# Performance work log

Measured on AMD Instinct MI355X. Metric: run time of the kernel, lower is better.

The kernel has to match this reference:

```python
import jax, jax.numpy as jnp
import numpy as np

N_NODES = 50000
N_EDGES = 800000
NUM_FEATS = 512
NUM_CLASSES = 64
NUM_LAYERS = 4


def setup_inputs() -> dict:
    key = jax.random.key(0)
    k1, k2, k3 = jax.random.split(key, 3)
    x = jax.random.normal(k1, (N_NODES, NUM_FEATS), dtype=jnp.float32)
    # glorot init for weight [num_feats, num_classes]
    scale = jnp.sqrt(6.0 / (NUM_FEATS + NUM_CLASSES)).astype(jnp.float32)
    weight = jax.random.uniform(k2, (NUM_FEATS, NUM_CLASSES), dtype=jnp.float32,
                                minval=-scale, maxval=scale)
    edge_index = jax.random.randint(k3, (2, N_EDGES), 0, N_NODES, dtype=jnp.int64)
    return {"x": x, "weight": weight, "edge_index": edge_index}


def reference(x, weight, edge_index):
    row, col = edge_index[0], edge_index[1]  # [E], [E]
    # symmetric GCN normalization: deg^{-1/2}[row] * deg^{-1/2}[col]
    deg = jax.ops.segment_sum(jnp.ones((edge_index.shape[1],), dtype=x.dtype),
                              row, num_segments=x.shape[0])  # [N]
    deg_inv_sqrt = jnp.where(deg > 0, jax.lax.rsqrt(jnp.maximum(deg, 1e-12)), 0.0)
    norm = (deg_inv_sqrt[row] * deg_inv_sqrt[col])[:, None]  # [E, 1]

    h = x @ weight  # [N, num_classes] (dropout skipped: eval mode)
    for _ in range(NUM_LAYERS):
        # gather source features, scale by edge norm, scatter-add to destinations
        msg = norm * h[row]  # [E, num_classes]
        h = jax.ops.segment_sum(msg, col, num_segments=x.shape[0])  # [N, num_classes]
        # type_norm == 'None' -> layers_bn is identity
    return h
```

## Files before the change

kernel.cpp:

```cpp
#include <hip/hip_runtime.h>
#include <hip/hip_fp16.h>

#define NFEAT 512
#define NCLS  64
#define NNODES 50000
#define NW    (NNODES / 4)
#define NB    256
#define SLOTS 64

typedef unsigned int uint;
using short8 = __attribute__((ext_vector_type(8))) short;
using f32x4  = __attribute__((ext_vector_type(4))) float;

static __device__ __forceinline__ unsigned short f32_to_bf16_rne(float f) {
    unsigned u = __float_as_uint(f);
    unsigned r = u + 0x7FFFu + ((u >> 16) & 1u);
    return (unsigned short)(r >> 16);
}
static __device__ __forceinline__ float bf16_to_f32(unsigned short b) {
    return __uint_as_float(((unsigned)b) << 16);
}
static __device__ __forceinline__ uint cvt_pk_bf16(float a, float b) {
    uint r;
    asm("v_cvt_pk_bf16_f32 %0, %1, %2" : "=v"(r) : "v"(a), "v"(b));
    return r;
}
static __device__ __forceinline__ void split_bf16x8(const float* xs, short8& ahi, short8& alo) {
    union { uint u[4]; short8 s; } H, L;
#pragma unroll
    for (int t = 0; t < 4; ++t) {
        float x0 = xs[2 * t], x1 = xs[2 * t + 1];
        uint hp = cvt_pk_bf16(x0, x1);
        float f0 = __uint_as_float(hp << 16);
        float f1 = __uint_as_float(hp & 0xffff0000u);
        uint lp = cvt_pk_bf16(x0 - f0, x1 - f1);
        H.u[t] = hp; L.u[t] = lp;
    }
    ahi = H.s; alo = L.s;
}


__global__ __launch_bounds__(256) void hist_packw_kernel(
        const int* __restrict__ row, const int* __restrict__ col,
        const float* __restrict__ w,
        uint* __restrict__ degB, uint* __restrict__ cntB,
        short8* __restrict__ wp, int E, int CH) {
    __shared__ __align__(16) uint h[2 * NW];
    int b = blockIdx.x;
    if (b < NB) {
        for (int i = threadIdx.x; i < 2 * NW; i += 256) h[i] = 0;
        __syncthreads();
        int e0 = b * CH, e1 = min(E, e0 + CH);
        for (int e = e0 + threadIdx.x; e < e1; e += 256) {
            int c = col[e], r = row[e];
            atomicAdd(&h[c >> 2], 1u << ((c & 3) * 8));
            atomicAdd(&h[NW + (r >> 2)], 1u << ((r & 3) * 8));
        }
        __syncthreads();
        uint4* cb = reinterpret_cast<uint4*>(cntB + (size_t)b * NW);
        uint4* db = reinterpret_cast<uint4*>(degB + (size_t)b * NW);
        const uint4* c4 = reinterpret_cast<const uint4*>(h);
        const uint4* d4 = reinterpret_cast<const uint4*>(h + NW);
        for (int i = threadIdx.x; i < NW / 4; i += 256) cb[i] = c4[i];
        for (int i = threadIdx.x; i < NW / 4; i += 256) db[i] = d4[i];
        return;
    }
    int gid = (b - NB) * 256 + threadIdx.x;
    int lane = gid & 63;
    int F = gid >> 6;
    int s = F & 1;
    int nt = (F >> 1) & 3;
    int kk = F >> 3;
    int k0 = kk * 32 + (lane >> 4) * 8;
    int c  = nt * 16 + (lane & 15);
    short8 v;
#pragma unroll
    for (int j = 0; j < 8; ++j) {
        float xv = w[(k0 + j) * NCLS + c];
        unsigned short hi = f32_to_bf16_rne(xv);
        unsigned short outv = hi;
        if (s) outv = f32_to_bf16_rne(xv - bf16_to_f32(hi));
        v[j] = (short)outv;
    }
    wp[gid] = v;
}


__global__ __launch_bounds__(256) void reduce_kernel(uint* __restrict__ cntB,
                                                     const uint* __restrict__ degB,
                                                     int* __restrict__ cntTot,
                                                     float* __restrict__ dinv) {
    int gid = blockIdx.x * 256 + threadIdx.x;
    if (gid < NW) {
        int wi = gid;
        uint run = 0;
#pragma unroll 8
        for (int b = 0; b < NB; ++b) {
            uint v = cntB[(size_t)b * NW + wi];
            cntB[(size_t)b * NW + wi] = run;
            run += v;
        }
        int4 t = { (int)(run & 255), (int)((run >> 8) & 255),
                   (int)((run >> 16) & 255), (int)(run >> 24) };
        *reinterpret_cast<int4*>(cntTot + wi * 4) = t;
    } else if (gid < 2 * NW) {
        int wi = gid - NW;
        uint run = 0;
#pragma unroll 8
        for (int b = 0; b < NB; ++b) run += degB[(size_t)b * NW + wi];
        int d0 = run & 255, d1 = (run >> 8) & 255, d2 = (run >> 16) & 255, d3 = run >> 24;
        float4 dv;
        dv.x = d0 ? rsqrtf((float)d0) : 0.0f;
        dv.y = d1 ? rsqrtf((float)d1) : 0.0f;
        dv.z = d2 ? rsqrtf((float)d2) : 0.0f;
        dv.w = d3 ? rsqrtf((float)d3) : 0.0f;
        *reinterpret_cast<float4*>(dinv + wi * 4) = dv;
    }
}


__global__ __launch_bounds__(256, 2) void place_matmul_kernel(
        const int* __restrict__ row, const int* __restrict__ col,
        const uint* __restrict__ offB, int* __restrict__ slots,
        const float* __restrict__ x, const short8* __restrict__ wp,
        const float* __restrict__ dinv, __half* __restrict__ u0,
        int N, int E, int CH) {
    __shared__ __align__(16) uint sh[NW];
    int b = blockIdx.x;

    if (b < NB) {
        uint4* c4 = reinterpret_cast<uint4*>(sh);
        const uint4* o4 = reinterpret_cast<const uint4*>(offB + (size_t)b * NW);
        for (int i = threadIdx.x; i < NW / 4; i += 256) c4[i] = o4[i];
        __syncthreads();
        int e0 = b * CH, e1 = min(E, e0 + CH);
        for (int e = e0 + threadIdx.x; e < e1; e += 256) {
            int c = col[e];
            uint old = atomicAdd(&sh[c >> 2], 1u << ((c & 3) * 8));
            int pos = (old >> ((c & 3) * 8)) & 255;
            if (pos < SLOTS) slots[(c << 6) + pos] = row[e];
        }
        return;
    }

    int tile = b - NB;
    int tid = threadIdx.x;
    int wave = tid >> 6, lane = tid & 63;
    int rlo = lane & 15, khi = lane >> 4;
    int row0 = tile * 128 + wave * 32;

    size_t roff[2];
#pragma unroll
    for (int rg = 0; rg < 2; ++rg) {
        int rr = row0 + rg * 16 + rlo;
        if (rr > N - 1) rr = N - 1;
        roff[rg] = (size_t)rr * NFEAT + khi * 8;
    }

    f32x4 acc[2][4];
#pragma unroll
    for (int rg = 0; rg < 2; ++rg)
#pragma unroll
        for (int nt = 0; nt < 4; ++nt) acc[rg][nt] = f32x4{0.f, 0.f, 0.f, 0.f};

    const short8* fbase = wp + lane;
    for (int ch = 0; ch < 4; ++ch) {
#pragma unroll
        for (int kk = 0; kk < 4; ++kk) {
            const short8* fb = fbase + ch * 2048 + kk * 512;
            short8 bh0 = fb[0],   bl0 = fb[64];
            short8 bh1 = fb[128], bl1 = fb[192];
            short8 bh2 = fb[256], bl2 = fb[320];
            short8 bh3 = fb[384], bl3 = fb[448];
            int kg = ch * 128 + kk * 32;
#pragma unroll
            for (int rg = 0; rg < 2; ++rg) {
                float4 xa = *reinterpret_cast<const float4*>(x + roff[rg] + kg);
                float4 xb = *reinterpret_cast<const float4*>(x + roff[rg] + kg + 4);
                float xs[8] = {xa.x, xa.y, xa.z, xa.w, xb.x, xb.y, xb.z, xb.w};
                short8 ahi, alo;
                split_bf16x8(xs, ahi, alo);
                acc[rg][0] = __builtin_amdgcn_mfma_f32_16x16x32_bf16(ahi, bh0, acc[rg][0], 0, 0, 0);
                acc[rg][1] = __builtin_amdgcn_mfma_f32_16x16x32_bf16(ahi, bh1, acc[rg][1], 0, 0, 0);
                acc[rg][2] = __builtin_amdgcn_mfma_f32_16x16x32_bf16(ahi, bh2, acc[rg][2], 0, 0, 0);
                acc[rg][3] = __builtin_amdgcn_mfma_f32_16x16x32_bf16(ahi, bh3, acc[rg][3], 0, 0, 0);
                acc[rg][0] = __builtin_amdgcn_mfma_f32_16x16x32_bf16(alo, bh0, acc[rg][0], 0, 0, 0);
                acc[rg][1] = __builtin_amdgcn_mfma_f32_16x16x32_bf16(alo, bh1, acc[rg][1], 0, 0, 0);
                acc[rg][2] = __builtin_amdgcn_mfma_f32_16x16x32_bf16(alo, bh2, acc[rg][2], 0, 0, 0);
                acc[rg][3] = __builtin_amdgcn_mfma_f32_16x16x32_bf16(alo, bh3, acc[rg][3], 0, 0, 0);
                acc[rg][0] = __builtin_amdgcn_mfma_f32_16x16x32_bf16(ahi, bl0, acc[rg][0], 0, 0, 0);
                acc[rg][1] = __builtin_amdgcn_mfma_f32_16x16x32_bf16(ahi, bl1, acc[rg][1], 0, 0, 0);
                acc[rg][2] = __builtin_amdgcn_mfma_f32_16x16x32_bf16(ahi, bl2, acc[rg][2], 0, 0, 0);
                acc[rg][3] = __builtin_amdgcn_mfma_f32_16x16x32_bf16(ahi, bl3, acc[rg][3], 0, 0, 0);
            }
        }
    }

#pragma unroll
    for (int rg = 0; rg < 2; ++rg) {
        int rbase = row0 + rg * 16 + khi * 4;
#pragma unroll
        for (int j = 0; j < 4; ++j) {
            int r = rbase + j;
            if (r < N) {
                float dn = dinv[r];
                __half* op = u0 + ((size_t)r << 6) + rlo;
                op[0]  = __float2half(acc[rg][0][j] * dn);
                op[16] = __float2half(acc[rg][1][j] * dn);
                op[32] = __float2half(acc[rg][2][j] * dn);
                op[48] = __float2half(acc[rg][3][j] * dn);
            }
        }
    }
}


__global__ __launch_bounds__(256) void gather_kernel(const __half* __restrict__ u,
                                                     const int* __restrict__ cntTot,
                                                     const int* __restrict__ slots,
                                                     const float* __restrict__ dinv,
                                                     __half* __restrict__ out_h,
                                                     float* __restrict__ out_f,
                                                     int N, int sq) {
    int wid = blockIdx.x * 4 + (threadIdx.x >> 6);
    if (wid >= N) return;
    int lane = threadIdx.x & 63;
    int q = lane >> 3;
    int p = lane & 7;
    int cq = cntTot[wid];
    cq = (cq < SLOTS) ? cq : SLOTS;
    const int* sl = slots + (wid << 6);
    int s_l = sl[lane];

    float a0=0.f,a1=0.f,a2=0.f,a3=0.f,a4=0.f,a5=0.f,a6=0.f,a7=0.f;
    float b0=0.f,b1=0.f,b2=0.f,b3=0.f,b4=0.f,b5=0.f,b6=0.f,b7=0.f;
#pragma unroll
    for (int j = 0; j < 8; j += 2) {
        int i0 = q + 8 * j;
        int i1 = q + 8 * (j + 1);
        int s0 = __shfl(s_l, i0);
        int s1 = __shfl(s_l, i1);
        if (i0 < cq) {
            uint4 d0 = *reinterpret_cast<const uint4*>(u + ((size_t)s0 << 6) + p * 8);
            float2 f0 = __half22float2(*reinterpret_cast<__half2*>(&d0.x));
            float2 f1 = __half22float2(*reinterpret_cast<__half2*>(&d0.y));
            float2 f2 = __half22float2(*reinterpret_cast<__half2*>(&d0.z));
            float2 f3 = __half22float2(*reinterpret_cast<__half2*>(&d0.w));
            a0 += f0.x; a1 += f0.y; a2 += f1.x; a3 += f1.y;
            a4 += f2.x; a5 += f2.y; a6 += f3.x; a7 += f3.y;
        }
        if (i1 < cq) {
            uint4 d1 = *reinterpret_cast<const uint4*>(u + ((size_t)s1 << 6) + p * 8);
            float2 g0 = __half22float2(*reinterpret_cast<__half2*>(&d1.x));
            float2 g1 = __half22float2(*reinterpret_cast<__half2*>(&d1.y));
            float2 g2 = __half22float2(*reinterpret_cast<__half2*>(&d1.z));
            float2 g3 = __half22float2(*reinterpret_cast<__half2*>(&d1.w));
            b0 += g0.x; b1 += g0.y; b2 += g1.x; b3 += g1.y;
            b4 += g2.x; b5 += g2.y; b6 += g3.x; b7 += g3.y;
        }
    }
    a0 += b0; a1 += b1; a2 += b2; a3 += b3;
    a4 += b4; a5 += b5; a6 += b6; a7 += b7;
#pragma unroll
    for (int off = 8; off < 64; off <<= 1) {
        a0 += __shfl_xor(a0, off); a1 += __shfl_xor(a1, off);
        a2 += __shfl_xor(a2, off); a3 += __shfl_xor(a3, off);
        a4 += __shfl_xor(a4, off); a5 += __shfl_xor(a5, off);
        a6 += __shfl_xor(a6, off); a7 += __shfl_xor(a7, off);
    }
    if (q == 0) {
        float sc = dinv[wid];
        if (sq) {
            sc *= sc;
            __half2 h0 = __floats2half2_rn(a0 * sc, a1 * sc);
            __half2 h1 = __floats2half2_rn(a2 * sc, a3 * sc);
            __half2 h2 = __floats2half2_rn(a4 * sc, a5 * sc);
            __half2 h3 = __floats2half2_rn(a6 * sc, a7 * sc);
            uint4 d;
            d.x = *reinterpret_cast<uint*>(&h0);
            d.y = *reinterpret_cast<uint*>(&h1);
            d.z = *reinterpret_cast<uint*>(&h2);
            d.w = *reinterpret_cast<uint*>(&h3);
            *reinterpret_cast<uint4*>(out_h + ((size_t)wid << 6) + p * 8) = d;
        } else {
            float4 r0 = {a0 * sc, a1 * sc, a2 * sc, a3 * sc};
            float4 r1 = {a4 * sc, a5 * sc, a6 * sc, a7 * sc};
            float4* op = reinterpret_cast<float4*>(out_f + ((size_t)wid << 6) + p * 8);
            op[0] = r0;
            op[1] = r1;
        }
    }
}


extern "C" void kernel_launch(void* const* d_in, const int* in_sizes, int n_in,
                              void* d_out, int out_size, void* d_ws, size_t ws_size,
                              hipStream_t stream) {
    const float* x = (const float*)d_in[0];
    const float* w = (const float*)d_in[1];
    const int*   ei = (const int*)d_in[2];

    int N = in_sizes[0] / NFEAT;
    int E = in_sizes[2] / 2;
    const int* row = ei;
    const int* col = ei + E;
    float* out = (float*)d_out;

    auto align256 = [](size_t v) { return (v + 255) & ~(size_t)255; };
    char* ws = (char*)d_ws;
    size_t off = 0;
    uint* cntB   = (uint*)(ws + off);   off += align256((size_t)NB * NW * sizeof(uint));
    uint* degB   = (uint*)(ws + off);   off += align256((size_t)NB * NW * sizeof(uint));
    int* cntTot  = (int*)(ws + off);    off += align256((size_t)NNODES * sizeof(int));
    float* dinv  = (float*)(ws + off);  off += align256((size_t)NNODES * sizeof(float));
    short8* wp   = (short8*)(ws + off); off += align256((size_t)8192 * sizeof(short8));
    int* slots   = (int*)(ws + off);    off += align256((size_t)NNODES * SLOTS * sizeof(int));
    __half* uA   = (__half*)(ws + off); off += align256((size_t)NNODES * NCLS * sizeof(__half));
    __half* uB   = (__half*)(ws + off); off += align256((size_t)NNODES * NCLS * sizeof(__half));

    int CH = (E + NB - 1) / NB;

    hist_packw_kernel<<<NB + 32, 256, 0, stream>>>(row, col, w, degB, cntB, wp, E, CH);
    reduce_kernel<<<(2 * NW + 255) / 256, 256, 0, stream>>>(cntB, degB, cntTot, dinv);
    int nmm = (N + 127) / 128;
    place_matmul_kernel<<<NB + nmm, 256, 0, stream>>>(row, col, cntB, slots,
                                                      x, wp, dinv, uA, N, E, CH);

    int ngrid = (N + 3) / 4;
    gather_kernel<<<ngrid, 256, 0, stream>>>(uA, cntTot, slots, dinv, uB, nullptr, N, 1);
    gather_kernel<<<ngrid, 256, 0, stream>>>(uB, cntTot, slots, dinv, uA, nullptr, N, 1);
    gather_kernel<<<ngrid, 256, 0, stream>>>(uA, cntTot, slots, dinv, uB, nullptr, N, 1);
    gather_kernel<<<ngrid, 256, 0, stream>>>(uB, cntTot, slots, dinv, nullptr, out, N, 0);
}
```

Before: 158.6 us.

## Split placement from matmul, add per-node slot sorting, prefetch x rows

Moves the edge placement into its own kernel so the matmul no longer reserves the large shared-memory histogram, letting the matmul run at higher occupancy with smaller 64-row tiles and a software prefetch of the next x chunk. The freed matmul launch also gets extra blocks that bitonic-sort each node's source-index slots with wave shuffles, presumably to make later gathers more cache-friendly and the summation order deterministic. This adds a kernel launch and sort work, and the placement no longer overlaps with the matmul.

```diff
diff --git a/kernel.cpp b/kernel.cpp
--- a/kernel.cpp
+++ b/kernel.cpp
@@ -119,97 +119,117 @@
 }
 
 
-__global__ __launch_bounds__(256, 2) void place_matmul_kernel(
+__global__ __launch_bounds__(256) void place_kernel(
         const int* __restrict__ row, const int* __restrict__ col,
         const uint* __restrict__ offB, int* __restrict__ slots,
+        int E, int CH) {
+    __shared__ __align__(16) uint sh[NW];
+    int b = blockIdx.x;
+    uint4* c4 = reinterpret_cast<uint4*>(sh);
+    const uint4* o4 = reinterpret_cast<const uint4*>(offB + (size_t)b * NW);
+    for (int i = threadIdx.x; i < NW / 4; i += 256) c4[i] = o4[i];
+    __syncthreads();
+    int e0 = b * CH, e1 = min(E, e0 + CH);
+    for (int e = e0 + threadIdx.x; e < e1; e += 256) {
+        int c = col[e];
+        uint old = atomicAdd(&sh[c >> 2], 1u << ((c & 3) * 8));
+        int pos = (old >> ((c & 3) * 8)) & 255;
+        if (pos < SLOTS) slots[(c << 6) + pos] = row[e];
+    }
+}
+
+
+__global__ __launch_bounds__(256, 4) void matmul_sort_kernel(
         const float* __restrict__ x, const short8* __restrict__ wp,
         const float* __restrict__ dinv, __half* __restrict__ u0,
-        int N, int E, int CH) {
-    __shared__ __align__(16) uint sh[NW];
+        int* __restrict__ slots, const int* __restrict__ cntTot,
+        int N, int nmm) {
     int b = blockIdx.x;
-
-    if (b < NB) {
-        uint4* c4 = reinterpret_cast<uint4*>(sh);
-        const uint4* o4 = reinterpret_cast<const uint4*>(offB + (size_t)b * NW);
-        for (int i = threadIdx.x; i < NW / 4; i += 256) c4[i] = o4[i];
-        __syncthreads();
-        int e0 = b * CH, e1 = min(E, e0 + CH);
-        for (int e = e0 + threadIdx.x; e < e1; e += 256) {
-            int c = col[e];
-            uint old = atomicAdd(&sh[c >> 2], 1u << ((c & 3) * 8));
-            int pos = (old >> ((c & 3) * 8)) & 255;
-            if (pos < SLOTS) slots[(c << 6) + pos] = row[e];
-        }
-        return;
-    }
-
-    int tile = b - NB;
     int tid = threadIdx.x;
     int wave = tid >> 6, lane = tid & 63;
+
+    if (b >= nmm) {
+        int base = (b - nmm) * 16 + wave * 4;
+#pragma unroll
+        for (int k = 0; k < 4; ++k) {
+            int wid = base + k;
+            if (wid >= N) break;
+            int cq = cntTot[wid];
+            cq = (cq < SLOTS) ? cq : SLOTS;
+            int* sl = slots + (wid << 6);
+            int v = (lane < cq) ? sl[lane] : 0x7fffffff;
+#pragma unroll
+            for (int kk = 2; kk <= 64; kk <<= 1) {
+#pragma unroll
+                for (int j = kk >> 1; j >= 1; j >>= 1) {
+                    int p = __shfl_xor(v, j);
+                    int lo = min(v, p), hi = max(v, p);
+                    bool up = ((lane & kk) == 0);
+                    v = (((lane & j) == 0) == up) ? lo : hi;
+                }
+            }
+            if (lane < cq) sl[lane] = v;
+        }
+        return;
+    }
+
     int rlo = lane & 15, khi = lane >> 4;
-    int row0 = tile * 128 + wave * 32;
-
-    size_t roff[2];
-#pragma unroll
-    for (int rg = 0; rg < 2; ++rg) {
-        int rr = row0 + rg * 16 + rlo;
-        if (rr > N - 1) rr = N - 1;
-        roff[rg] = (size_t)rr * NFEAT + khi * 8;
-    }
-
-    f32x4 acc[2][4];
-#pragma unroll
-    for (int rg = 0; rg < 2; ++rg)
-#pragma unroll
-        for (int nt = 0; nt < 4; ++nt) acc[rg][nt] = f32x4{0.f, 0.f, 0.f, 0.f};
+    int row0 = b * 64 + wave * 16;
+    int rn = row0 + rlo; if (rn > N - 1) rn = N - 1;
+    const float* xr = x + (size_t)rn * NFEAT + khi * 8;
+
+    f32x4 acc[4];
+#pragma unroll
+    for (int nt = 0; nt < 4; ++nt) acc[nt] = f32x4{0.f, 0.f, 0.f, 0.f};
 
     const short8* fbase = wp + lane;
-    for (int ch = 0; ch < 4; ++ch) {
-#pragma unroll
-        for (int kk = 0; kk < 4; ++kk) {
-            const short8* fb = fbase + ch * 2048 + kk * 512;
-            short8 bh0 = fb[0],   bl0 = fb[64];
-            short8 bh1 = fb[128], bl1 = fb[192];
-            short8 bh2 = fb[256], bl2 = fb[320];
-            short8 bh3 = fb[384], bl3 = fb[448];
-            int kg = ch * 128 + kk * 32;
-#pragma unroll
-            for (int rg = 0; rg < 2; ++rg) {
-                float4 xa = *reinterpret_cast<const float4*>(x + roff[rg] + kg);
-                float4 xb = *reinterpret_cast<const float4*>(x + roff[rg] + kg + 4);
-                float xs[8] = {xa.x, xa.y, xa.z, xa.w, xb.x, xb.y, xb.z, xb.w};
-                short8 ahi, alo;
-                split_bf16x8(xs, ahi, alo);
-                acc[rg][0] = __builtin_amdgcn_mfma_f32_16x16x32_bf16(ahi, bh0, acc[rg][0], 0, 0, 0);
-                acc[rg][1] = __builtin_amdgcn_mfma_f32_16x16x32_bf16(ahi, bh1, acc[rg][1], 0, 0, 0);
-                acc[rg][2] = __builtin_amdgcn_mfma_f32_16x16x32_bf16(ahi, bh2, acc[rg][2], 0, 0, 0);
-                acc[rg][3] = __builtin_amdgcn_mfma_f32_16x16x32_bf16(ahi, bh3, acc[rg][3], 0, 0, 0);
-                acc[rg][0] = __builtin_amdgcn_mfma_f32_16x16x32_bf16(alo, bh0, acc[rg][0], 0, 0, 0);
-                acc[rg][1] = __builtin_amdgcn_mfma_f32_16x16x32_bf16(alo, bh1, acc[rg][1], 0, 0, 0);
-                acc[rg][2] = __builtin_amdgcn_mfma_f32_16x16x32_bf16(alo, bh2, acc[rg][2], 0, 0, 0);
-                acc[rg][3] = __builtin_amdgcn_mfma_f32_16x16x32_bf16(alo, bh3, acc[rg][3], 0, 0, 0);
-                acc[rg][0] = __builtin_amdgcn_mfma_f32_16x16x32_bf16(ahi, bl0, acc[rg][0], 0, 0, 0);
-                acc[rg][1] = __builtin_amdgcn_mfma_f32_16x16x32_bf16(ahi, bl1, acc[rg][1], 0, 0, 0);
-                acc[rg][2] = __builtin_amdgcn_mfma_f32_16x16x32_bf16(ahi, bl2, acc[rg][2], 0, 0, 0);
-                acc[rg][3] = __builtin_amdgcn_mfma_f32_16x16x32_bf16(ahi, bl3, acc[rg][3], 0, 0, 0);
-            }
-        }
-    }
-
-#pragma unroll
-    for (int rg = 0; rg < 2; ++rg) {
-        int rbase = row0 + rg * 16 + khi * 4;
-#pragma unroll
-        for (int j = 0; j < 4; ++j) {
-            int r = rbase + j;
-            if (r < N) {
-                float dn = dinv[r];
-                __half* op = u0 + ((size_t)r << 6) + rlo;
-                op[0]  = __float2half(acc[rg][0][j] * dn);
-                op[16] = __float2half(acc[rg][1][j] * dn);
-                op[32] = __float2half(acc[rg][2][j] * dn);
-                op[48] = __float2half(acc[rg][3][j] * dn);
-            }
+    float4 xa = *reinterpret_cast<const float4*>(xr);
+    float4 xb = *reinterpret_cast<const float4*>(xr + 4);
+
+#pragma unroll
+    for (int it = 0; it < 16; ++it) {
+        const short8* fb = fbase + it * 512;
+        short8 bf0 = fb[0],   bf1 = fb[64];
+        short8 bf2 = fb[128], bf3 = fb[192];
+        short8 bf4 = fb[256], bf5 = fb[320];
+        short8 bf6 = fb[384], bf7 = fb[448];
+
+        float4 nxa, nxb;
+        if (it < 15) {
+            nxa = *reinterpret_cast<const float4*>(xr + (it + 1) * 32);
+            nxb = *reinterpret_cast<const float4*>(xr + (it + 1) * 32 + 4);
+        }
+
+        float xs[8] = {xa.x, xa.y, xa.z, xa.w, xb.x, xb.y, xb.z, xb.w};
+        short8 ahi, alo;
+        split_bf16x8(xs, ahi, alo);
+        acc[0] = __builtin_amdgcn_mfma_f32_16x16x32_bf16(ahi, bf0, acc[0], 0, 0, 0);
+        acc[1] = __builtin_amdgcn_mfma_f32_16x16x32_bf16(ahi, bf2, acc[1], 0, 0, 0);
+        acc[2] = __builtin_amdgcn_mfma_f32_16x16x32_bf16(ahi, bf4, acc[2], 0, 0, 0);
+        acc[3] = __builtin_amdgcn_mfma_f32_16x16x32_bf16(ahi, bf6, acc[3], 0, 0, 0);
+        acc[0] = __builtin_amdgcn_mfma_f32_16x16x32_bf16(alo, bf0, acc[0], 0, 0, 0);
+        acc[1] = __builtin_amdgcn_mfma_f32_16x16x32_bf16(alo, bf2, acc[1], 0, 0, 0);
+        acc[2] = __builtin_amdgcn_mfma_f32_16x16x32_bf16(alo, bf4, acc[2], 0, 0, 0);
+        acc[3] = __builtin_amdgcn_mfma_f32_16x16x32_bf16(alo, bf6, acc[3], 0, 0, 0);
+        acc[0] = __builtin_amdgcn_mfma_f32_16x16x32_bf16(ahi, bf1, acc[0], 0, 0, 0);
+        acc[1] = __builtin_amdgcn_mfma_f32_16x16x32_bf16(ahi, bf3, acc[1], 0, 0, 0);
+        acc[2] = __builtin_amdgcn_mfma_f32_16x16x32_bf16(ahi, bf5, acc[2], 0, 0, 0);
+        acc[3] = __builtin_amdgcn_mfma_f32_16x16x32_bf16(ahi, bf7, acc[3], 0, 0, 0);
+
+        if (it < 15) { xa = nxa; xb = nxb; }
+    }
+
+    int rbase = row0 + khi * 4;
+#pragma unroll
+    for (int j = 0; j < 4; ++j) {
+        int r = rbase + j;
+        if (r < N) {
+            float dn = dinv[r];
+            __half* op = u0 + ((size_t)r << 6) + rlo;
+            op[0]  = __float2half(acc[0][j] * dn);
+            op[16] = __float2half(acc[1][j] * dn);
+            op[32] = __float2half(acc[2][j] * dn);
+            op[48] = __float2half(acc[3][j] * dn);
         }
     }
 }
@@ -322,9 +342,11 @@
 
     hist_packw_kernel<<<NB + 32, 256, 0, stream>>>(row, col, w, degB, cntB, wp, E, CH);
     reduce_kernel<<<(2 * NW + 255) / 256, 256, 0, stream>>>(cntB, degB, cntTot, dinv);
-    int nmm = (N + 127) / 128;
-    place_matmul_kernel<<<NB + nmm, 256, 0, stream>>>(row, col, cntB, slots,
-                                                      x, wp, dinv, uA, N, E, CH);
+    place_kernel<<<NB, 256, 0, stream>>>(row, col, cntB, slots, E, CH);
+    int nmm = (N + 63) / 64;
+    int nsort = (N + 15) / 16;
+    matmul_sort_kernel<<<nmm + nsort, 256, 0, stream>>>(x, wp, dinv, uA,
+                                                        slots, cntTot, N, nmm);
 
     int ngrid = (N + 3) / 4;
     gather_kernel<<<ngrid, 256, 0, stream>>>(uA, cntTot, slots, dinv, uB, nullptr, N, 1);
```

Measured after the change: 174.6 us. +10.1%, slower.

## Split per-node count scan into two levels and sort neighbor slots in first gather

Applied to the files above, without the earlier changes.

The serial 256-step column scan over per-block histograms becomes two stages. Eight sub-scans of 32 blocks each run in parallel, then a small top-level scan combines the sub-totals and produces dinv and total counts. The placement kernel adds the sub-group offset when loading its per-block offsets. The first gather pass also bitonic-sorts each node's neighbor slot list within the wave and writes it back, so later passes read neighbor rows in ascending index order for better locality. The cost is an extra launch, extra workspace traffic, and sort work in one gather.

```diff
diff --git a/kernel.cpp b/kernel.cpp
--- a/kernel.cpp
+++ b/kernel.cpp
@@ -6,6 +6,7 @@
 #define NNODES 50000
 #define NW    (NNODES / 4)
 #define NB    256
+#define NG    8
 #define SLOTS 64
 
 typedef unsigned int uint;
@@ -86,42 +87,67 @@
 }
 
 
-__global__ __launch_bounds__(256) void reduce_kernel(uint* __restrict__ cntB,
-                                                     const uint* __restrict__ degB,
-                                                     int* __restrict__ cntTot,
-                                                     float* __restrict__ dinv) {
+__global__ __launch_bounds__(256) void scan_sub_kernel(uint* __restrict__ cntB,
+                                                       const uint* __restrict__ degB,
+                                                       uint* __restrict__ cntSub,
+                                                       uint* __restrict__ degSub) {
     int gid = blockIdx.x * 256 + threadIdx.x;
-    if (gid < NW) {
-        int wi = gid;
+    if (gid >= 2 * NG * NW) return;
+    int half = gid / (NG * NW);
+    int rem  = gid % (NG * NW);
+    int g = rem / NW, wi = rem % NW;
+    if (half == 0) {
         uint run = 0;
 #pragma unroll 8
-        for (int b = 0; b < NB; ++b) {
+        for (int b = g * 32; b < g * 32 + 32; ++b) {
             uint v = cntB[(size_t)b * NW + wi];
             cntB[(size_t)b * NW + wi] = run;
             run += v;
         }
-        int4 t = { (int)(run & 255), (int)((run >> 8) & 255),
-                   (int)((run >> 16) & 255), (int)(run >> 24) };
-        *reinterpret_cast<int4*>(cntTot + wi * 4) = t;
-    } else if (gid < 2 * NW) {
-        int wi = gid - NW;
+        cntSub[(size_t)g * NW + wi] = run;
+    } else {
         uint run = 0;
 #pragma unroll 8
-        for (int b = 0; b < NB; ++b) run += degB[(size_t)b * NW + wi];
-        int d0 = run & 255, d1 = (run >> 8) & 255, d2 = (run >> 16) & 255, d3 = run >> 24;
-        float4 dv;
-        dv.x = d0 ? rsqrtf((float)d0) : 0.0f;
-        dv.y = d1 ? rsqrtf((float)d1) : 0.0f;
-        dv.z = d2 ? rsqrtf((float)d2) : 0.0f;
-        dv.w = d3 ? rsqrtf((float)d3) : 0.0f;
-        *reinterpret_cast<float4*>(dinv + wi * 4) = dv;
-    }
+        for (int b = g * 32; b < g * 32 + 32; ++b) run += degB[(size_t)b * NW + wi];
+        degSub[(size_t)g * NW + wi] = run;
+    }
+}
+
+
+__global__ __launch_bounds__(256) void scan_top_kernel(uint* __restrict__ cntSub,
+                                                       const uint* __restrict__ degSub,
+                                                       int* __restrict__ cntTot,
+                                                       float* __restrict__ dinv) {
+    int wi = blockIdx.x * 256 + threadIdx.x;
+    if (wi >= NW) return;
+    uint run = 0;
+#pragma unroll
+    for (int g = 0; g < NG; ++g) {
+        uint v = cntSub[(size_t)g * NW + wi];
+        cntSub[(size_t)g * NW + wi] = run;
+        run += v;
+    }
+    int4 t = { (int)(run & 255), (int)((run >> 8) & 255),
+               (int)((run >> 16) & 255), (int)(run >> 24) };
+    *reinterpret_cast<int4*>(cntTot + wi * 4) = t;
+
+    uint run2 = 0;
+#pragma unroll
+    for (int g = 0; g < NG; ++g) run2 += degSub[(size_t)g * NW + wi];
+    int d0 = run2 & 255, d1 = (run2 >> 8) & 255, d2 = (run2 >> 16) & 255, d3 = run2 >> 24;
+    float4 dv;
+    dv.x = d0 ? rsqrtf((float)d0) : 0.0f;
+    dv.y = d1 ? rsqrtf((float)d1) : 0.0f;
+    dv.z = d2 ? rsqrtf((float)d2) : 0.0f;
+    dv.w = d3 ? rsqrtf((float)d3) : 0.0f;
+    *reinterpret_cast<float4*>(dinv + wi * 4) = dv;
 }
 
 
 __global__ __launch_bounds__(256, 2) void place_matmul_kernel(
         const int* __restrict__ row, const int* __restrict__ col,
-        const uint* __restrict__ offB, int* __restrict__ slots,
+        const uint* __restrict__ offB, const uint* __restrict__ cntSub,
+        int* __restrict__ slots,
         const float* __restrict__ x, const short8* __restrict__ wp,
         const float* __restrict__ dinv, __half* __restrict__ u0,
         int N, int E, int CH) {
@@ -131,7 +157,12 @@
     if (b < NB) {
         uint4* c4 = reinterpret_cast<uint4*>(sh);
         const uint4* o4 = reinterpret_cast<const uint4*>(offB + (size_t)b * NW);
-        for (int i = threadIdx.x; i < NW / 4; i += 256) c4[i] = o4[i];
+        const uint4* s4 = reinterpret_cast<const uint4*>(cntSub + (size_t)(b >> 5) * NW);
+        for (int i = threadIdx.x; i < NW / 4; i += 256) {
+            uint4 a = o4[i], d = s4[i];
+            a.x += d.x; a.y += d.y; a.z += d.z; a.w += d.w;
+            c4[i] = a;
+        }
         __syncthreads();
         int e0 = b * CH, e1 = min(E, e0 + CH);
         for (int e = e0 + threadIdx.x; e < e1; e += 256) {
@@ -217,11 +248,11 @@
 
 __global__ __launch_bounds__(256) void gather_kernel(const __half* __restrict__ u,
                                                      const int* __restrict__ cntTot,
-                                                     const int* __restrict__ slots,
+                                                     int* __restrict__ slots,
                                                      const float* __restrict__ dinv,
                                                      __half* __restrict__ out_h,
                                                      float* __restrict__ out_f,
-                                                     int N, int sq) {
+                                                     int N, int sq, int dosort) {
     int wid = blockIdx.x * 4 + (threadIdx.x >> 6);
     if (wid >= N) return;
     int lane = threadIdx.x & 63;
@@ -229,8 +260,24 @@
     int p = lane & 7;
     int cq = cntTot[wid];
     cq = (cq < SLOTS) ? cq : SLOTS;
-    const int* sl = slots + (wid << 6);
+    int* sl = slots + (wid << 6);
     int s_l = sl[lane];
+
+    if (dosort) {
+        int v = (lane < cq) ? s_l : 0x7fffffff;
+#pragma unroll
+        for (int k = 2; k <= 64; k <<= 1) {
+#pragma unroll
+            for (int j = k >> 1; j >= 1; j >>= 1) {
+                int pv = __shfl_xor(v, j);
+                int lo = min(v, pv), hi = max(v, pv);
+                bool up = ((lane & k) == 0);
+                v = (((lane & j) == 0) == up) ? lo : hi;
+            }
+        }
+        s_l = v;
+        if (lane < cq) sl[lane] = v;
+    }
 
     float a0=0.f,a1=0.f,a2=0.f,a3=0.f,a4=0.f,a5=0.f,a6=0.f,a7=0.f;
     float b0=0.f,b1=0.f,b2=0.f,b3=0.f,b4=0.f,b5=0.f,b6=0.f,b7=0.f;
@@ -311,6 +358,8 @@
     size_t off = 0;
     uint* cntB   = (uint*)(ws + off);   off += align256((size_t)NB * NW * sizeof(uint));
     uint* degB   = (uint*)(ws + off);   off += align256((size_t)NB * NW * sizeof(uint));
+    uint* cntSub = (uint*)(ws + off);   off += align256((size_t)NG * NW * sizeof(uint));
+    uint* degSub = (uint*)(ws + off);   off += align256((size_t)NG * NW * sizeof(uint));
     int* cntTot  = (int*)(ws + off);    off += align256((size_t)NNODES * sizeof(int));
     float* dinv  = (float*)(ws + off);  off += align256((size_t)NNODES * sizeof(float));
     short8* wp   = (short8*)(ws + off); off += align256((size_t)8192 * sizeof(short8));
@@ -321,14 +370,15 @@
     int CH = (E + NB - 1) / NB;
 
     hist_packw_kernel<<<NB + 32, 256, 0, stream>>>(row, col, w, degB, cntB, wp, E, CH);
-    reduce_kernel<<<(2 * NW + 255) / 256, 256, 0, stream>>>(cntB, degB, cntTot, dinv);
+    scan_sub_kernel<<<(2 * NG * NW + 255) / 256, 256, 0, stream>>>(cntB, degB, cntSub, degSub);
+    scan_top_kernel<<<(NW + 255) / 256, 256, 0, stream>>>(cntSub, degSub, cntTot, dinv);
     int nmm = (N + 127) / 128;
-    place_matmul_kernel<<<NB + nmm, 256, 0, stream>>>(row, col, cntB, slots,
+    place_matmul_kernel<<<NB + nmm, 256, 0, stream>>>(row, col, cntB, cntSub, slots,
                                                       x, wp, dinv, uA, N, E, CH);
 
     int ngrid = (N + 3) / 4;
-    gather_kernel<<<ngrid, 256, 0, stream>>>(uA, cntTot, slots, dinv, uB, nullptr, N, 1);
-    gather_kernel<<<ngrid, 256, 0, stream>>>(uB, cntTot, slots, dinv, uA, nullptr, N, 1);
-    gather_kernel<<<ngrid, 256, 0, stream>>>(uA, cntTot, slots, dinv, uB, nullptr, N, 1);
-    gather_kernel<<<ngrid, 256, 0, stream>>>(uB, cntTot, slots, dinv, nullptr, out, N, 0);
-}
+    gather_kernel<<<ngrid, 256, 0, stream>>>(uA, cntTot, slots, dinv, uB, nullptr, N, 1, 1);
+    gather_kernel<<<ngrid, 256, 0, stream>>>(uB, cntTot, slots, dinv, uA, nullptr, N, 1, 0);
+    gather_kernel<<<ngrid, 256, 0, stream>>>(uA, cntTot, slots, dinv, uB, nullptr, N, 1, 0);
+    gather_kernel<<<ngrid, 256, 0, stream>>>(uB, cntTot, slots, dinv, nullptr, out, N, 0, 0);
+}
```

Measured after the change: 160.6 us. About the same (+1.2%).
